# Performance work log

Hardware: AMD Instinct MI355X
Metric: run time of the kernel (lower is better)

The kernel has to match this reference:

```python
import jax, jax.numpy as jnp
import numpy as np

GRID_DIMS = (64, 64, 64)
GRID_LOWER = np.array([0.0, 0.0, 0.0], np.float32)
GRID_STEPS = np.array([0.015625, 0.015625, 0.015625], np.float32)
RADIUS = 0.03125
STENCIL = 2  # ceil(radius / step)


def _poly6(d2, h):
    # standard SPH poly6 smoothing kernel: 315/(64 pi h^9) (h^2 - d^2)^3, d <= h
    c = np.float32(315.0 / (64.0 * np.pi * h ** 9))
    return jnp.where(d2 <= h * h, c * (h * h - d2) ** 3, 0.0)


def particles2grid(locs, data, density):
    # locs [B,N,3], data [B,N,C], density [B,N] -> grid [B,X,Y,Z,C]
    B, N, _ = locs.shape
    C = data.shape[-1]
    X, Y, Z = GRID_DIMS
    dims = jnp.array(GRID_DIMS, jnp.int32)
    r = jnp.arange(-STENCIL, STENCIL + 1)
    offs = jnp.stack(jnp.meshgrid(r, r, r, indexing='ij'), -1).reshape(-1, 3)  # [K,3]
    base = jnp.floor((locs - GRID_LOWER) / GRID_STEPS).astype(jnp.int32)        # [B,N,3]
    cells = base[:, :, None, :] + offs                                          # [B,N,K,3]
    centers = GRID_LOWER + (cells.astype(locs.dtype) + 0.5) * GRID_STEPS
    d2 = jnp.sum((centers - locs[:, :, None, :]) ** 2, -1)                      # [B,N,K]
    w = _poly6(d2, RADIUS)
    w = jnp.where(jnp.all((cells >= 0) & (cells < dims), -1), w, 0.0)
    contrib = w[..., None] * (data / density[..., None])[:, :, None, :]         # [B,N,K,C]
    cells = jnp.clip(cells, 0, dims - 1)
    flat = (cells[..., 0] * Y + cells[..., 1]) * Z + cells[..., 2]              # [B,N,K]

    def splat(f, c):
        return jnp.zeros((X * Y * Z, C), data.dtype).at[f.reshape(-1)].add(c.reshape(-1, C))

    return jax.vmap(splat)(flat, contrib).reshape(B, X, Y, Z, C)


def grid2particles(grid, locs):
    # trilinear interpolation of grid [B,X,Y,Z,C] at particle locations [B,N,3]
    B, X, Y, Z, C = grid.shape
    dims = jnp.array([X, Y, Z], jnp.int32)
    pos = (locs - GRID_LOWER) / GRID_STEPS - 0.5                                # cell-center coords
    i0 = jnp.floor(pos).astype(jnp.int32)
    frac = pos - i0.astype(locs.dtype)
    gflat = grid.reshape(B, X * Y * Z, C)
    gather = jax.vmap(lambda g, f: g[f])                                        # [B,N] -> [B,N,C]
    out = jnp.zeros((B, locs.shape[1], C), grid.dtype)
    for dx in (0, 1):
        for dy in (0, 1):
            for dz in (0, 1):
                off = jnp.array([dx, dy, dz], jnp.int32)
                idx = i0 + off
                wd = jnp.where(off == 1, frac, 1.0 - frac)                      # [B,N,3]
                w = wd[..., 0] * wd[..., 1] * wd[..., 2]
                w = jnp.where(jnp.all((idx >= 0) & (idx < dims), -1), w, 0.0)
                idx = jnp.clip(idx, 0, dims - 1)
                flat = (idx[..., 0] * Y + idx[..., 1]) * Z + idx[..., 2]
                out = out + w[..., None] * gather(gflat, flat)
    return out


def conv3d(x, w, b):
    y = jax.lax.conv_general_dilated(x, w, (1, 1, 1), 'SAME',
                                     dimension_numbers=('NCDHW', 'OIDHW', 'NCDHW'))
    return y + b[None, :, None, None, None]


def prelu(x, a):
    return jnp.where(x >= 0, x, a * x)


def setup_inputs() -> dict:
    key = jax.random.key(0)
    ks = jax.random.split(key, 8)
    B, N = 2, 32768
    Cin, K, Cout = 4, 32, 4
    s = lambda fan: np.float32(1.0 / np.sqrt(fan * 27))
    return {
        'locs': jax.random.uniform(ks[0], (B, N, 3), jnp.float32),
        'data': jax.random.normal(ks[1], (B, N, Cin), jnp.float32),
        'density': jax.random.uniform(ks[2], (B, N), jnp.float32, 0.5, 1.5),
        'W0': jax.random.normal(ks[3], (K, Cin, 3, 3, 3), jnp.float32) * s(Cin),
        'b0': jnp.zeros((K,), jnp.float32),
        'W1': jax.random.normal(ks[4], (K, K, 3, 3, 3), jnp.float32) * s(K),
        'b1': jnp.zeros((K,), jnp.float32),
        'W2': jax.random.normal(ks[5], (K, K, 3, 3, 3), jnp.float32) * s(K),
        'b2': jnp.zeros((K,), jnp.float32),
        'W3': jax.random.normal(ks[6], (Cout, K, 3, 3, 3), jnp.float32) * s(K),
        'b3': jnp.zeros((Cout,), jnp.float32),
        'a0': jnp.full((1,), 0.25, jnp.float32),
        'a1': jnp.full((1,), 0.25, jnp.float32),
        'a2': jnp.full((1,), 0.25, jnp.float32),
    }


def reference(locs, data, density, W0, b0, W1, b1, W2, b2, W3, b3, a0, a1, a2):
    grid = particles2grid(locs, data, density)            # [B,X,Y,Z,Cin]
    g = jnp.transpose(grid, (0, 4, 1, 2, 3))              # NCDHW
    g = prelu(conv3d(g, W0, b0), a0)
    g = prelu(conv3d(g, W1, b1), a1)
    g = prelu(conv3d(g, W2, b2), a2)
    g = conv3d(g, W3, b3)
    g = jnp.transpose(g, (0, 2, 3, 4, 1))                 # [B,X,Y,Z,Cout]
    return grid2particles(g, locs)                        # [B,N,Cout]
```

## Files before the change

kernel.cpp:

```cpp
#include <hip/hip_runtime.h>

#define BATCH 2
#define NPART 32768
#define GD 64
#define NVOX (BATCH * GD * GD * GD)

typedef unsigned short ushortT;
typedef __attribute__((ext_vector_type(8))) short short8;
typedef __attribute__((ext_vector_type(16))) float float16;

__device__ __forceinline__ float poly6_c() {
    const double H9 = 1.0 / 35184372088832.0;
    return (float)(315.0 / (64.0 * 3.14159265358979323846 * H9));
}

__device__ __forceinline__ ushortT bf16_rne(float f) {
    unsigned int u = __float_as_uint(f);
    u = (u + 0x7fffu + ((u >> 16) & 1u)) >> 16;
    return (ushortT)u;
}

__device__ __forceinline__ int imax(int a, int b) { return a > b ? a : b; }
__device__ __forceinline__ int imin(int a, int b) { return a < b ? a : b; }

__device__ __forceinline__ void load_lds16(const void* g, void* l) {
    __builtin_amdgcn_global_load_lds(
        (const __attribute__((address_space(1))) void*)g,
        (__attribute__((address_space(3))) void*)l, 16, 0, 0);
}

__global__ __launch_bounds__(256) void prep_kernel(
    int* __restrict__ zp,
    const float* __restrict__ W0, const float* __restrict__ W1,
    const float* __restrict__ W2, const float* __restrict__ W3,
    short* __restrict__ Bp) {
    int bid = blockIdx.x, tid = threadIdx.x;
    if (bid < 513) {
        int t = bid * 256 + tid;
        if (t < 131088) zp[t] = 0;
        return;
    }
    int t = (bid - 513) * 256 + tid;
    if (t >= 176 * 512) return;
    int kt = t >> 9;
    int l = (t >> 3) & 63, j = t & 7;
    int n = l & 31, q = l >> 5;
    float v = 0.f;
    if (kt < 14) {
        int k = kt * 16 + 8 * q + j;
        int tap = k >> 3, ic = k & 7;
        if (tap < 27 && ic < 4) v = W0[(n * 4 + ic) * 27 + tap];
    } else {
        const float* W; int O, s;
        if (kt < 68)       { W = W1; O = 32; s = kt - 14; }
        else if (kt < 122) { W = W2; O = 32; s = kt - 68; }
        else               { W = W3; O = 4;  s = kt - 122; }
        int h = s / 27, ss = s - h * 27;
        int gI = ss / 3, dy = ss - gI * 3;
        int dx = gI / 3, dz = gI - dx * 3;
        int tap = dx * 9 + dy * 3 + dz;
        int ic = h * 16 + q * 8 + j;
        if (n < O) v = W[(n * 32 + ic) * 27 + tap];
    }
    Bp[t] = (short)bf16_rne(v);
}

__global__ __launch_bounds__(256) void bin_count_kernel(
    const float* __restrict__ locs, int* __restrict__ counts) {
    int t = blockIdx.x * blockDim.x + threadIdx.x;
    if (t >= BATCH * NPART) return;
    int b = t >> 15;
    int bx = ((int)floorf(locs[t * 3 + 0] * 64.0f)) >> 1;
    int by = ((int)floorf(locs[t * 3 + 1] * 64.0f)) >> 1;
    int bz = ((int)floorf(locs[t * 3 + 2] * 64.0f)) >> 1;
    atomicAdd(&counts[b * 32768 + ((bx * 32) + by) * 32 + bz], 1);
}

__global__ __launch_bounds__(256) void scanA_kernel(
    const int* __restrict__ counts, int* __restrict__ offsets,
    int* __restrict__ blockSum) {
    __shared__ int sh[256];
    int tid = threadIdx.x, g = blockIdx.x;
    int v = counts[g * 256 + tid];
    sh[tid] = v;
    __syncthreads();
    for (int off = 1; off < 256; off <<= 1) {
        int u = (tid >= off) ? sh[tid - off] : 0;
        __syncthreads();
        sh[tid] += u;
        __syncthreads();
    }
    offsets[g * 256 + tid] = sh[tid] - v;
    if (tid == 255) blockSum[g] = sh[255];
}

__global__ __launch_bounds__(256) void scanB_kernel(
    int* __restrict__ offsets, const int* __restrict__ blockSum) {
    __shared__ int sh[256];
    int tid = threadIdx.x, g = blockIdx.x;
    sh[tid] = (tid < g) ? blockSum[tid] : 0;
    __syncthreads();
    for (int off = 128; off > 0; off >>= 1) {
        if (tid < off) sh[tid] += sh[tid + off];
        __syncthreads();
    }
    offsets[g * 256 + tid] += sh[0];
    if (g == 255 && tid == 255) offsets[65536] = BATCH * NPART;
}

__global__ __launch_bounds__(256) void bin_scatter_kernel(
    const float* __restrict__ locs, const float* __restrict__ data,
    const float* __restrict__ density, const int* __restrict__ offsets,
    int* __restrict__ cursor, float* __restrict__ payload) {
    int t = blockIdx.x * blockDim.x + threadIdx.x;
    if (t >= BATCH * NPART) return;
    int b = t >> 15;
    float px = locs[t * 3 + 0];
    float py = locs[t * 3 + 1];
    float pz = locs[t * 3 + 2];
    int bx = ((int)floorf(px * 64.0f)) >> 1;
    int by = ((int)floorf(py * 64.0f)) >> 1;
    int bz = ((int)floorf(pz * 64.0f)) >> 1;
    int bb = b * 32768 + ((bx * 32) + by) * 32 + bz;
    int slot = atomicAdd(&cursor[bb], 1);
    int idx = offsets[bb] + slot;
    float inv_d = 1.0f / density[t];
    float4 p0 = {px, py, pz, data[t * 4 + 0] * inv_d};
    float4 p1 = {data[t * 4 + 1] * inv_d, data[t * 4 + 2] * inv_d,
                 data[t * 4 + 3] * inv_d, 0.f};
    *(float4*)(payload + idx * 8)     = p0;
    *(float4*)(payload + idx * 8 + 4) = p1;
}

__global__ __launch_bounds__(256) void splat_gather_kernel(
    const float* __restrict__ payload, const int* __restrict__ offsets,
    ushortT* __restrict__ g8) {
    __shared__ float plist[256 * 8];
    __shared__ int segS[36];
    __shared__ int segP[37];
    __shared__ int shTot[1];

    int wg = blockIdx.x;
    int sb = wg & 511, b = wg >> 9;
    int X0 = (sb >> 6) * 8, Y0 = ((sb >> 3) & 7) * 8, Z0 = (sb & 7) * 8;
    int tid = threadIdx.x;

    int bxlo = imax(0, (X0 - 2) >> 1), bxhi = imin(31, (X0 + 9) >> 1);
    int bylo = imax(0, (Y0 - 2) >> 1), byhi = imin(31, (Y0 + 9) >> 1);
    int bzlo = imax(0, (Z0 - 2) >> 1), bzhi = imin(31, (Z0 + 9) >> 1);
    int ny = byhi - bylo + 1;
    int ns = (bxhi - bxlo + 1) * ny;
    if (tid < ns) {
        int bx = bxlo + tid / ny, by = bylo + tid % ny;
        int row = b * 32768 + (bx * 32 + by) * 32;
        int s = offsets[row + bzlo];
        int e = offsets[row + bzhi + 1];
        segS[tid] = s;
        segP[tid] = e - s;
    }
    __syncthreads();
    if (tid == 0) {
        int p = 0;
        for (int k = 0; k < ns; ++k) { int len = segP[k]; segP[k] = p; p += len; }
        segP[ns] = p;
        shTot[0] = p;
    }
    __syncthreads();

    const float step = 0.015625f;
    const float h2 = 0.03125f * 0.03125f;
    const float cc = poly6_c();
    int total = shTot[0];

    int l = tid & 63, w = tid >> 6;
    int cx = X0 + 4 * (w >> 1) + (l >> 4);
    int cy = Y0 + 4 * (w & 1) + ((l >> 2) & 3);
    int cz0 = Z0 + (l & 3);
    float xc  = ((float)cx  + 0.5f) * step;
    float yc  = ((float)cy  + 0.5f) * step;
    float zc0 = ((float)cz0 + 0.5f) * step;
    float zc1 = zc0 + 4.0f * step;

    float a00 = 0.f, a01 = 0.f, a02 = 0.f, a03 = 0.f;
    float a10 = 0.f, a11 = 0.f, a12 = 0.f, a13 = 0.f;

    int nchunks = (total + 255) >> 8;
    for (int ch = 0; ch < nchunks; ++ch) {
        __syncthreads();
        int jj = (ch << 8) + tid;
        if (jj < total) {
            int k = 0;
            while (jj >= segP[k + 1]) ++k;
            int idx = segS[k] + (jj - segP[k]);
            *(float4*)(plist + tid * 8)     = *(const float4*)(payload + idx * 8);
            *(float4*)(plist + tid * 8 + 4) = *(const float4*)(payload + idx * 8 + 4);
        }
        __syncthreads();
        int cnt = imin(256, total - (ch << 8));
        for (int p = 0; p < cnt; ++p) {
            float4 pa = *(const float4*)(plist + p * 8);
            float dx = pa.x - xc, dy = pa.y - yc;
            float dxy2 = fmaf(dy, dy, dx * dx);
            if (!__any(dxy2 <= h2)) continue;
            float4 pv = *(const float4*)(plist + p * 8 + 4);
            float dz0 = pa.z - zc0;
            float d20 = fmaf(dz0, dz0, dxy2);
            float u0 = fmaxf(h2 - d20, 0.f);
            float w0 = (cc * u0) * (u0 * u0);
            a00 = fmaf(w0, pa.w, a00);
            a01 = fmaf(w0, pv.x, a01);
            a02 = fmaf(w0, pv.y, a02);
            a03 = fmaf(w0, pv.z, a03);
            float dz1 = pa.z - zc1;
            float d21 = fmaf(dz1, dz1, dxy2);
            float u1 = fmaxf(h2 - d21, 0.f);
            float w1 = (cc * u1) * (u1 * u1);
            a10 = fmaf(w1, pa.w, a10);
            a11 = fmaf(w1, pv.x, a11);
            a12 = fmaf(w1, pv.y, a12);
            a13 = fmaf(w1, pv.z, a13);
        }
    }

    size_t cellBase = (size_t)(((b * 64 + cx) * 64 + cy) * 64);
    short8 o;
    o[0] = (short)bf16_rne(a00); o[1] = (short)bf16_rne(a01);
    o[2] = (short)bf16_rne(a02); o[3] = (short)bf16_rne(a03);
    o[4] = 0; o[5] = 0; o[6] = 0; o[7] = 0;
    *(short8*)(g8 + (cellBase + cz0) * 8) = o;
    o[0] = (short)bf16_rne(a10); o[1] = (short)bf16_rne(a11);
    o[2] = (short)bf16_rne(a12); o[3] = (short)bf16_rne(a13);
    *(short8*)(g8 + (cellBase + cz0 + 4) * 8) = o;
}

template <int ICG, int KT, bool FINAL>
__global__ __launch_bounds__(256, 2) void mfma_conv_kernel(
    const ushortT* __restrict__ in, const short* __restrict__ Bpack,
    const float* __restrict__ bias, const float* __restrict__ alpha,
    const float* __restrict__ zguard, void* __restrict__ outv) {
    constexpr int CIN  = ICG * 8;
    constexpr int NCHP = (ICG == 1) ? (24 * 34) : (24 * 2 * 34);
    constexpr int ABUF = NCHP * 8;
    constexpr int BKT  = (ICG == 1) ? KT : 27;
    constexpr int BBUF = BKT * 512;
    __shared__ short lds[2 * ABUF + BBUF];

    int wg = ((blockIdx.x & 7) << 7) | (blockIdx.x >> 3);
    int yq = wg & 15, xp = (wg >> 4) & 31, b = wg >> 9;
    int X0 = xp * 2, Y0 = yq * 4;
    int tid = threadIdx.x;
    const ushortT* inb = in + (size_t)b * (64 * 64 * 64 * CIN);

    int l = tid & 63, w = tid >> 6;
    int wx = w >> 1, wy2 = (w & 1) * 2;
    int n = l & 31, q = l >> 5;
    int laneZ = (l & 31) * 8;
    float bval = FINAL ? (n < 4 ? bias[n] : 0.f) : bias[n];
    const short* Bl = lds + 2 * ABUF;

    auto stageA = [&](int p) {
        int h, t;
        if constexpr (ICG == 1) { h = 0; t = p; } else { h = p >> 1; t = p & 1; }
        int zb = t * 32;
        short* dst = lds + (p & 1) * ABUF;
#pragma unroll
        for (int it = 0; it < (NCHP + 255) / 256; ++it) {
            int ccid = it * 256 + tid;
            if (ccid < NCHP) {
                int col, icg2, zi;
                if constexpr (ICG == 1) {
                    col = ccid / 34; zi = ccid - col * 34; icg2 = 0;
                } else {
                    col = ccid / 68;
                    int rem = ccid - col * 68;
                    icg2 = rem / 34; zi = rem - icg2 * 34;
                }
                int gx = X0 + col / 6 - 1;
                int gy = Y0 + col % 6 - 1;
                int gz = zb + zi - 1;
                const void* src = (const void*)zguard;
                if ((unsigned)gx < 64u && (unsigned)gy < 64u && (unsigned)gz < 64u)
                    src = (const void*)(inb +
                        ((size_t)(((gx * 64) + gy) * 64 + gz)) * CIN + (h * 2 + icg2) * 8);
                load_lds16(src, (void*)(dst + ccid * 8));
            }
        }
    };

    auto loadB = [&](int h) {
        const short* src0 = Bpack + (size_t)h * BBUF;
        short* dst = lds + 2 * ABUF;
        constexpr int NB = BBUF / 8;
#pragma unroll
        for (int it = 0; it < (NB + 255) / 256; ++it) {
            int ccid = it * 256 + tid;
            if (ccid < NB)
                load_lds16((const void*)(src0 + ccid * 8), (void*)(dst + ccid * 8));
        }
    };

    auto computeP = [&](int p, float16& c0, float16& c1) {
        const short* lb = lds + (p & 1) * ABUF;
        if constexpr (ICG == 1) {
#pragma unroll
            for (int kt = 0; kt < KT; ++kt) {
                short8 bcur = *(const short8*)(Bl + kt * 512 + l * 8);
                int tap0 = kt * 2, tap1 = kt * 2 + 1;
                if (tap1 > 26) tap1 = 26;
                int dx0 = tap0 / 9, r0 = tap0 - dx0 * 9, dy0 = r0 / 3, dz0 = r0 - dy0 * 3;
                int dx1 = tap1 / 9, r1 = tap1 - dx1 * 9, dy1 = r1 / 3, dz1 = r1 - dy1 * 3;
#define AOFS1(c) (q ? ((((wx + dx1) * 6 + ((c) + dy1)) * 34 + dz1) * 8) \
                    : ((((wx + dx0) * 6 + ((c) + dy0)) * 34 + dz0) * 8))
                short8 a0 = *(const short8*)(lb + AOFS1(wy2) + laneZ);
                short8 a1 = *(const short8*)(lb + AOFS1(wy2 + 1) + laneZ);
#undef AOFS1
                c0 = __builtin_amdgcn_mfma_f32_32x32x16_bf16(a0, bcur, c0, 0, 0, 0);
                c1 = __builtin_amdgcn_mfma_f32_32x32x16_bf16(a1, bcur, c1, 0, 0, 0);
            }
        } else {
#pragma unroll
            for (int g = 0; g < 9; ++g) {
                int dx = g / 3, dz = g - dx * 3;
                short8 fr[4];
#pragma unroll
                for (int k = 0; k < 4; ++k) {
                    int ofs = ((((wx + dx) * 6 + (wy2 + k)) * 2 + q) * 34 + dz) * 8;
                    fr[k] = *(const short8*)(lb + ofs + laneZ);
                }
#pragma unroll
                for (int dy = 0; dy < 3; ++dy) {
                    short8 bcur = *(const short8*)(Bl + (g * 3 + dy) * 512 + l * 8);
                    c0 = __builtin_amdgcn_mfma_f32_32x32x16_bf16(fr[0 + dy], bcur, c0, 0, 0, 0);
                    c1 = __builtin_amdgcn_mfma_f32_32x32x16_bf16(fr[1 + dy], bcur, c1, 0, 0, 0);
                }
            }
        }
    };

    auto epi = [&](int t, const float16& c0, const float16& c1) {
        int Z0 = t * 32;
        size_t base0 = (size_t)(((b * 64 + X0 + wx) * 64 + (Y0 + wy2)) * 64) + Z0;
        if constexpr (FINAL) {
            float* out = (float*)outv;
            if (n < 4) {
#pragma unroll
                for (int r = 0; r < 16; ++r) {
                    int z = (r & 3) + 8 * (r >> 2) + 4 * q;
                    out[(base0 + z) * 4 + n]      = c0[r];
                    out[(base0 + 64 + z) * 4 + n] = c1[r];
                }
            }
        } else {
            float a = alpha[0];
            ushortT* out = (ushortT*)outv;
#pragma unroll
            for (int r = 0; r < 16; ++r) {
                int z = (r & 3) + 8 * (r >> 2) + 4 * q;
                float v0 = c0[r]; v0 = v0 >= 0.f ? v0 : a * v0;
                out[(base0 + z) * 32 + n] = bf16_rne(v0);
                float v1 = c1[r]; v1 = v1 >= 0.f ? v1 : a * v1;
                out[(base0 + 64 + z) * 32 + n] = bf16_rne(v1);
            }
        }
    };

    float16 a00, a01, a10, a11;
#pragma unroll
    for (int r = 0; r < 16; ++r) {
        a00[r] = bval; a01[r] = bval; a10[r] = bval; a11[r] = bval;
    }

    stageA(0);
    loadB(0);

    if constexpr (ICG == 1) {
        __syncthreads();
        stageA(1);
        computeP(0, a00, a01);
        epi(0, a00, a01);
        __syncthreads();
        computeP(1, a10, a11);
        epi(1, a10, a11);
    } else {
        __syncthreads();
        stageA(1);
        computeP(0, a00, a01);
        __syncthreads();
        stageA(2);
        computeP(1, a10, a11);
        __syncthreads();
        loadB(1);
        __syncthreads();
        stageA(3);
        computeP(2, a00, a01);
        epi(0, a00, a01);
        __syncthreads();
        computeP(3, a10, a11);
        epi(1, a10, a11);
    }
}

__global__ __launch_bounds__(256) void gather_kernel(
    const float* __restrict__ grid, const float* __restrict__ locs,
    float* __restrict__ out) {
    int t = blockIdx.x * blockDim.x + threadIdx.x;
    if (t >= BATCH * NPART) return;
    int b = t >> 15;

    float px = locs[t * 3 + 0] * 64.0f - 0.5f;
    float py = locs[t * 3 + 1] * 64.0f - 0.5f;
    float pz = locs[t * 3 + 2] * 64.0f - 0.5f;
    int ix = (int)floorf(px);
    int iy = (int)floorf(py);
    int iz = (int)floorf(pz);
    float fx = px - (float)ix;
    float fy = py - (float)iy;
    float fz = pz - (float)iz;

    const float* gb = grid + (size_t)b * GD * GD * GD * 4;
    float o0 = 0.f, o1 = 0.f, o2 = 0.f, o3 = 0.f;

#pragma unroll
    for (int dx = 0; dx < 2; ++dx) {
        int x = ix + dx;
        if ((unsigned)x > 63u) continue;
        float wx = dx ? fx : 1.0f - fx;
#pragma unroll
        for (int dy = 0; dy < 2; ++dy) {
            int y = iy + dy;
            if ((unsigned)y > 63u) continue;
            float wy = dy ? fy : 1.0f - fy;
#pragma unroll
            for (int dz = 0; dz < 2; ++dz) {
                int z = iz + dz;
                if ((unsigned)z > 63u) continue;
                float wz = dz ? fz : 1.0f - fz;
                float w = wx * wy * wz;
                const float4 g = *(const float4*)(gb + (size_t)(((x * GD) + y) * GD + z) * 4);
                o0 += w * g.x; o1 += w * g.y; o2 += w * g.z; o3 += w * g.w;
            }
        }
    }
    out[t * 4 + 0] = o0;
    out[t * 4 + 1] = o1;
    out[t * 4 + 2] = o2;
    out[t * 4 + 3] = o3;
}

extern "C" void kernel_launch(void* const* d_in, const int* in_sizes, int n_in,
                              void* d_out, int out_size, void* d_ws, size_t ws_size,
                              hipStream_t stream) {
    const float* locs    = (const float*)d_in[0];
    const float* data    = (const float*)d_in[1];
    const float* density = (const float*)d_in[2];
    const float* W0 = (const float*)d_in[3];
    const float* b0 = (const float*)d_in[4];
    const float* W1 = (const float*)d_in[5];
    const float* b1 = (const float*)d_in[6];
    const float* W2 = (const float*)d_in[7];
    const float* b2 = (const float*)d_in[8];
    const float* W3 = (const float*)d_in[9];
    const float* b3 = (const float*)d_in[10];
    const float* a0 = (const float*)d_in[11];
    const float* a1 = (const float*)d_in[12];
    const float* a2 = (const float*)d_in[13];
    float* out = (float*)d_out;

    char* ws = (char*)d_ws;
    ushortT* g8  = (ushortT*)(ws);
    ushortT* gA  = (ushortT*)(ws + 8388608);
    ushortT* gB  = (ushortT*)(ws + 41943040);
    float*  gF   = (float*)(ws + 75497472);
    short*  Bp   = (short*)(ws + 83886080);
    short*  Bp0  = Bp;
    short*  Bp1  = Bp + 14 * 512;
    short*  Bp2  = Bp + 68 * 512;
    short*  Bp3  = Bp + 122 * 512;
    float* zguard   = (float*)(ws + 84066240);
    int*   counts   = (int*)(ws + 84066304);
    int*   cursor   = (int*)(ws + 84328448);
    int*   offsets  = (int*)(ws + 84590592);
    int*   blockSum = (int*)(ws + 84852752);
    float* payload  = (float*)(ws + 84853888);

    prep_kernel<<<513 + 352, 256, 0, stream>>>((int*)zguard, W0, W1, W2, W3, Bp);

    bin_count_kernel<<<(BATCH * NPART) / 256, 256, 0, stream>>>(locs, counts);
    scanA_kernel<<<256, 256, 0, stream>>>(counts, offsets, blockSum);
    scanB_kernel<<<256, 256, 0, stream>>>(offsets, blockSum);
    bin_scatter_kernel<<<(BATCH * NPART) / 256, 256, 0, stream>>>(
        locs, data, density, offsets, cursor, payload);

    splat_gather_kernel<<<BATCH * 512, 256, 0, stream>>>(payload, offsets, g8);

    const int CGRID = 1024;
    mfma_conv_kernel< 1, 14, false><<<CGRID, 256, 0, stream>>>(g8, Bp0, b0, a0, zguard, gA);
    mfma_conv_kernel< 4, 54, false><<<CGRID, 256, 0, stream>>>(gA, Bp1, b1, a1, zguard, gB);
    mfma_conv_kernel< 4, 54, false><<<CGRID, 256, 0, stream>>>(gB, Bp2, b2, a2, zguard, gA);
    mfma_conv_kernel< 4, 54, true ><<<CGRID, 256, 0, stream>>>(gA, Bp3, b3, b3, zguard, gF);

    gather_kernel<<<(BATCH * NPART) / 256, 256, 0, stream>>>(gF, locs, out);
}
```

Measured before the change: 239.8 us.

## Keep weights in registers and triple-buffer activation staging with counted waits

Weight fragments are now loaded straight from global memory into per-lane registers instead of being staged through LDS, which frees LDS for a third activation buffer in the multi-group conv. Each wave stages its own quarter of the input tile, and full __syncthreads are replaced by explicit vmcnt waits plus barriers, so the next stage's loads can stay in flight while the current stage computes. MFMA issue is wrapped in s_setprio to favour the matrix work. The risks are much higher register pressure from holding up to 27 short8 weight fragments, which could spill or lower occupancy under launch_bounds(256,2). The hand-counted vmcnt values must also match the number of outstanding loads exactly, or the kernel will read stale data.

```diff
diff --git a/kernel.cpp b/kernel.cpp
--- a/kernel.cpp
+++ b/kernel.cpp
@@ -28,6 +28,13 @@
         (const __attribute__((address_space(1))) void*)g,
         (__attribute__((address_space(3))) void*)l, 16, 0, 0);
 }
+
+#define PWAIT(N) do {                                            \
+    asm volatile("s_waitcnt vmcnt(" #N ")" ::: "memory");        \
+    __builtin_amdgcn_sched_barrier(0);                           \
+    __builtin_amdgcn_s_barrier();                                \
+    __builtin_amdgcn_sched_barrier(0);                           \
+} while (0)
 
 __global__ __launch_bounds__(256) void prep_kernel(
     int* __restrict__ zp,
@@ -240,10 +247,12 @@
     const float* __restrict__ zguard, void* __restrict__ outv) {
     constexpr int CIN  = ICG * 8;
     constexpr int NCHP = (ICG == 1) ? (24 * 34) : (24 * 2 * 34);
-    constexpr int ABUF = NCHP * 8;
-    constexpr int BKT  = (ICG == 1) ? KT : 27;
-    constexpr int BBUF = BKT * 512;
-    __shared__ short lds[2 * ABUF + BBUF];
+    constexpr int PERW = NCHP / 4;
+    constexpr int NV   = (PERW + 63) / 64;
+    constexpr int BUFS = NCHP * 8;
+    constexpr int NBUF = (ICG == 1) ? 2 : 3;
+    constexpr int NBH  = (ICG == 1) ? KT : 27;
+    __shared__ short lds[NBUF * BUFS];
 
     int wg = ((blockIdx.x & 7) << 7) | (blockIdx.x >> 3);
     int yq = wg & 15, xp = (wg >> 4) & 31, b = wg >> 9;
@@ -255,18 +264,19 @@
     int wx = w >> 1, wy2 = (w & 1) * 2;
     int n = l & 31, q = l >> 5;
     int laneZ = (l & 31) * 8;
+    const short* bp = Bpack + (size_t)l * 8;
     float bval = FINAL ? (n < 4 ? bias[n] : 0.f) : bias[n];
-    const short* Bl = lds + 2 * ABUF;
 
     auto stageA = [&](int p) {
-        int h, t;
-        if constexpr (ICG == 1) { h = 0; t = p; } else { h = p >> 1; t = p & 1; }
+        int t = (ICG == 1) ? p : (p & 1);
+        int h = (ICG == 1) ? 0 : (p >> 1);
         int zb = t * 32;
-        short* dst = lds + (p & 1) * ABUF;
-#pragma unroll
-        for (int it = 0; it < (NCHP + 255) / 256; ++it) {
-            int ccid = it * 256 + tid;
-            if (ccid < NCHP) {
+        short* dst = lds + (p % NBUF) * BUFS;
+#pragma unroll
+        for (int it = 0; it < NV; ++it) {
+            int idx = it * 64 + l;
+            if (idx < PERW) {
+                int ccid = w * PERW + idx;
                 int col, icg2, zi;
                 if constexpr (ICG == 1) {
                     col = ccid / 34; zi = ccid - col * 34; icg2 = 0;
@@ -287,53 +297,46 @@
         }
     };
 
-    auto loadB = [&](int h) {
-        const short* src0 = Bpack + (size_t)h * BBUF;
-        short* dst = lds + 2 * ABUF;
-        constexpr int NB = BBUF / 8;
-#pragma unroll
-        for (int it = 0; it < (NB + 255) / 256; ++it) {
-            int ccid = it * 256 + tid;
-            if (ccid < NB)
-                load_lds16((const void*)(src0 + ccid * 8), (void*)(dst + ccid * 8));
+    short8 bh[NBH];
+
+    auto compute4 = [&](const short* lb, float16& c0, float16& c1) {
+#pragma unroll
+        for (int g = 0; g < 9; ++g) {
+            int dxg = g / 3, dzg = g - dxg * 3;
+            short8 fr[4];
+#pragma unroll
+            for (int k = 0; k < 4; ++k) {
+                int ofs = ((((wx + dxg) * 6 + (wy2 + k)) * 2 + q) * 34 + dzg) * 8;
+                fr[k] = *(const short8*)(lb + ofs + laneZ);
+            }
+#pragma unroll
+            for (int dy = 0; dy < 3; ++dy) {
+                short8 bcur = bh[g * 3 + dy];
+                __builtin_amdgcn_s_setprio(1);
+                c0 = __builtin_amdgcn_mfma_f32_32x32x16_bf16(fr[0 + dy], bcur, c0, 0, 0, 0);
+                c1 = __builtin_amdgcn_mfma_f32_32x32x16_bf16(fr[1 + dy], bcur, c1, 0, 0, 0);
+                __builtin_amdgcn_s_setprio(0);
+            }
         }
     };
 
-    auto computeP = [&](int p, float16& c0, float16& c1) {
-        const short* lb = lds + (p & 1) * ABUF;
-        if constexpr (ICG == 1) {
-#pragma unroll
-            for (int kt = 0; kt < KT; ++kt) {
-                short8 bcur = *(const short8*)(Bl + kt * 512 + l * 8);
-                int tap0 = kt * 2, tap1 = kt * 2 + 1;
-                if (tap1 > 26) tap1 = 26;
-                int dx0 = tap0 / 9, r0 = tap0 - dx0 * 9, dy0 = r0 / 3, dz0 = r0 - dy0 * 3;
-                int dx1 = tap1 / 9, r1 = tap1 - dx1 * 9, dy1 = r1 / 3, dz1 = r1 - dy1 * 3;
+    auto compute1 = [&](const short* lb, float16& c0, float16& c1) {
+#pragma unroll
+        for (int kt = 0; kt < KT; ++kt) {
+            short8 bcur = bh[kt];
+            int tap0 = kt * 2, tap1 = kt * 2 + 1;
+            if (tap1 > 26) tap1 = 26;
+            int dx0 = tap0 / 9, r0 = tap0 - dx0 * 9, dy0 = r0 / 3, dz0 = r0 - dy0 * 3;
+            int dx1 = tap1 / 9, r1 = tap1 - dx1 * 9, dy1 = r1 / 3, dz1 = r1 - dy1 * 3;
 #define AOFS1(c) (q ? ((((wx + dx1) * 6 + ((c) + dy1)) * 34 + dz1) * 8) \
                     : ((((wx + dx0) * 6 + ((c) + dy0)) * 34 + dz0) * 8))
-                short8 a0 = *(const short8*)(lb + AOFS1(wy2) + laneZ);
-                short8 a1 = *(const short8*)(lb + AOFS1(wy2 + 1) + laneZ);
+            short8 a0 = *(const short8*)(lb + AOFS1(wy2) + laneZ);
+            short8 a1 = *(const short8*)(lb + AOFS1(wy2 + 1) + laneZ);
 #undef AOFS1
-                c0 = __builtin_amdgcn_mfma_f32_32x32x16_bf16(a0, bcur, c0, 0, 0, 0);
-                c1 = __builtin_amdgcn_mfma_f32_32x32x16_bf16(a1, bcur, c1, 0, 0, 0);
-            }
-        } else {
-#pragma unroll
-            for (int g = 0; g < 9; ++g) {
-                int dx = g / 3, dz = g - dx * 3;
-                short8 fr[4];
-#pragma unroll
-                for (int k = 0; k < 4; ++k) {
-                    int ofs = ((((wx + dx) * 6 + (wy2 + k)) * 2 + q) * 34 + dz) * 8;
-                    fr[k] = *(const short8*)(lb + ofs + laneZ);
-                }
-#pragma unroll
-                for (int dy = 0; dy < 3; ++dy) {
-                    short8 bcur = *(const short8*)(Bl + (g * 3 + dy) * 512 + l * 8);
-                    c0 = __builtin_amdgcn_mfma_f32_32x32x16_bf16(fr[0 + dy], bcur, c0, 0, 0, 0);
-                    c1 = __builtin_amdgcn_mfma_f32_32x32x16_bf16(fr[1 + dy], bcur, c1, 0, 0, 0);
-                }
-            }
+            __builtin_amdgcn_s_setprio(1);
+            c0 = __builtin_amdgcn_mfma_f32_32x32x16_bf16(a0, bcur, c0, 0, 0, 0);
+            c1 = __builtin_amdgcn_mfma_f32_32x32x16_bf16(a1, bcur, c1, 0, 0, 0);
+            __builtin_amdgcn_s_setprio(0);
         }
     };
 
@@ -364,39 +367,42 @@
         }
     };
 
-    float16 a00, a01, a10, a11;
-#pragma unroll
-    for (int r = 0; r < 16; ++r) {
-        a00[r] = bval; a01[r] = bval; a10[r] = bval; a11[r] = bval;
-    }
-
-    stageA(0);
-    loadB(0);
-
     if constexpr (ICG == 1) {
-        __syncthreads();
+        float16 c00, c01, c10, c11;
+#pragma unroll
+        for (int r = 0; r < 16; ++r) { c00[r] = bval; c01[r] = bval; c10[r] = bval; c11[r] = bval; }
+#pragma unroll
+        for (int i = 0; i < NBH; ++i) bh[i] = *(const short8*)(bp + i * 512);
+        stageA(0);
         stageA(1);
-        computeP(0, a00, a01);
-        epi(0, a00, a01);
-        __syncthreads();
-        computeP(1, a10, a11);
-        epi(1, a10, a11);
+        PWAIT(4);
+        compute1(lds + 0 * BUFS, c00, c01);
+        epi(0, c00, c01);
+        PWAIT(0);
+        compute1(lds + 1 * BUFS, c10, c11);
+        epi(1, c10, c11);
     } else {
-        __syncthreads();
+        float16 c00, c01, c10, c11;
+#pragma unroll
+        for (int r = 0; r < 16; ++r) { c00[r] = bval; c01[r] = bval; c10[r] = bval; c11[r] = bval; }
+#pragma unroll
+        for (int i = 0; i < NBH; ++i) bh[i] = *(const short8*)(bp + i * 512);
+        stageA(0);
         stageA(1);
-        computeP(0, a00, a01);
-        __syncthreads();
+        PWAIT(7);
         stageA(2);
-        computeP(1, a10, a11);
-        __syncthreads();
-        loadB(1);
-        __syncthreads();
+        compute4(lds + 0 * BUFS, c00, c01);
+        PWAIT(7);
         stageA(3);
-        computeP(2, a00, a01);
-        epi(0, a00, a01);
-        __syncthreads();
-        computeP(3, a10, a11);
-        epi(1, a10, a11);
+        compute4(lds + 1 * BUFS, c10, c11);
+#pragma unroll
+        for (int i = 0; i < NBH; ++i) bh[i] = *(const short8*)(bp + (27 + i) * 512);
+        PWAIT(7);
+        compute4(lds + 2 * BUFS, c00, c01);
+        epi(0, c00, c01);
+        PWAIT(0);
+        compute4(lds + 0 * BUFS, c10, c11);
+        epi(1, c10, c11);
     }
 }
 
```

Result: slower. 279.7 us (+16.7%).
